# Kernel optimization log

Measured on AMD Instinct MI355X. Metric: run time of the kernel, lower is better.

## Reference

```python
import jax, jax.numpy as jnp
import numpy as np

DEPTH = 9                 # complete binary tree depth
N = 2 ** (DEPTH + 1) - 1  # 1023 nodes per tree (heap layout)
B = 32                    # batch of trees
E = 256                   # word_emb_dims
H = 512                   # treelstm in_dim (cell hidden size)
L = 512                   # decoder LSTM dims
V = 32000                 # vocab size
T = 64                    # max_sequence_length (greedy decode steps)


def setup_inputs() -> dict:
    key = jax.random.key(0)
    ks = jax.random.split(key, 12)
    g = lambda i, shape, s=0.02: jax.random.normal(ks[i], shape, jnp.float32) * s
    return {
        "node_feat": jax.random.randint(ks[0], (B, N), 0, V),
        "mask": jnp.ones((B, N), jnp.int32),
        # shared token embedding (node_emb_layer token_emb, also used by decoder input)
        "emb": g(1, (V, E)),
        # ChildSumTreeLSTMCell params (DGL convention)
        "W_iou": g(2, (E, 3 * H)),
        "U_iou": g(3, (H, 3 * H)),
        "b_iou": jnp.zeros((3 * H,), jnp.float32),
        "U_f_w": g(4, (H, H)),
        "U_f_b": jnp.zeros((H,), jnp.float32),
        # graph-readout -> decoder init state projections
        "hid_fc_w": g(5, (H, L)), "hid_fc_b": jnp.zeros((L,), jnp.float32),
        "cell_fc_w": g(6, (H, L)), "cell_fc_b": jnp.zeros((L,), jnp.float32),
        # decoder LSTMCell (PyTorch gate order i,f,g,o) + vocab projection
        "W_ih": g(7, (E, 4 * L)), "W_hh": g(8, (L, 4 * L)),
        "b_ih": jnp.zeros((4 * L,), jnp.float32), "b_hh": jnp.zeros((4 * L,), jnp.float32),
        "fc_w": g(9, (L, V)), "fc_b": jnp.zeros((V,), jnp.float32),
    }


def _forward(node_feat, mask, emb, W_iou, U_iou, b_iou, U_f_w, U_f_b,
             hid_fc_w, hid_fc_b, cell_fc_w, cell_fc_b,
             W_ih, W_hh, b_ih, b_hh, fc_w, fc_b):
    x = emb[node_feat]                                        # [B,N,E]
    iou_in = (x @ W_iou) * mask[..., None].astype(x.dtype)    # [B,N,3H]
    h = jnp.zeros((B, N, H), x.dtype)
    c = jnp.zeros((B, N, H), x.dtype)

    def apply_node(iou_node, c_agg):
        i, o, u = jnp.split(iou_node + b_iou, 3, axis=-1)
        i, o, u = jax.nn.sigmoid(i), jax.nn.sigmoid(o), jnp.tanh(u)
        c_new = i * u + c_agg
        return o * jnp.tanh(c_new), c_new

    # leaves first (no children -> zero aggregated cell)
    leaf = jnp.arange(2 ** DEPTH - 1, N)
    h_l, c_l = apply_node(iou_in[:, leaf], jnp.zeros((), x.dtype))
    h = h.at[:, leaf].set(h_l)
    c = c.at[:, leaf].set(c_l)

    # level-batched topological propagation (dgl.prop_nodes_topo)
    for d in range(DEPTH - 1, -1, -1):
        idx = jnp.arange(2 ** d - 1, 2 ** (d + 1) - 1)        # nodes at level d
        ch = jnp.stack([2 * idx + 1, 2 * idx + 2], axis=1)    # [n_d,2]
        h_ch, c_ch = h[:, ch], c[:, ch]                       # [B,n_d,2,H]
        h_tild = h_ch.sum(2)                                  # child-sum
        f = jax.nn.sigmoid(h_ch @ U_f_w + U_f_b)              # per-child forget gate
        c_agg = (f * c_ch).sum(2)
        h_n, c_n = apply_node(iou_in[:, idx] + h_tild @ U_iou, c_agg)
        h = h.at[:, idx].set(h_n)
        c = c.at[:, idx].set(c_n)

    mean_feats = h.mean(1)                                    # mean graph readout [B,H]
    hid = mean_feats @ hid_fc_w + hid_fc_b
    cel = mean_feats @ cell_fc_w + cell_fc_b

    def step(carry, _):
        inp, hs, cs = carry
        xt = emb[inp]                                         # [B,E]
        gates = xt @ W_ih + hs @ W_hh + b_ih + b_hh
        ig, fg, gg, og = jnp.split(gates, 4, axis=-1)
        cs = jax.nn.sigmoid(fg) * cs + jax.nn.sigmoid(ig) * jnp.tanh(gg)
        hs = jax.nn.sigmoid(og) * jnp.tanh(cs)
        logits = hs @ fc_w + fc_b                             # [B,V]
        top1 = jnp.argmax(logits, axis=-1)                    # greedy feedback
        return (top1, hs, cs), logits

    inp0 = jnp.zeros((B,), node_feat.dtype)
    _, logits_seq = jax.lax.scan(step, (inp0, hid, cel), None, length=T - 1)
    # t=0 row stays zeros, matching logits_output initialization
    return jnp.concatenate([jnp.zeros((1, B, V), x.dtype), logits_seq], axis=0)


def reference(node_feat, mask, emb, W_iou, U_iou, b_iou, U_f_w, U_f_b,
              hid_fc_w, hid_fc_b, cell_fc_w, cell_fc_b,
              W_ih, W_hh, b_ih, b_hh, fc_w, fc_b):
    return _forward(node_feat, mask, emb, W_iou, U_iou, b_iou, U_f_w, U_f_b,
                    hid_fc_w, hid_fc_b, cell_fc_w, cell_fc_b,
                    W_ih, W_hh, b_ih, b_hh, fc_w, fc_b)
```

## Files before the change

kernel.cpp:

```cpp
#include <hip/hip_runtime.h>
#include <math.h>

#define B_ 32
#define N_ 1023
#define E_ 256
#define H_ 512
#define V_ 32000
#define T_ 64
#define NBL 250

__device__ __forceinline__ float sigf(float x) { return 1.0f / (1.0f + expf(-x)); }

template<bool LEAF>
__global__ void __launch_bounds__(256)
iou_gemm_k(const int* __restrict__ node_feat, const int* __restrict__ mask,
           const float* __restrict__ emb, const float* __restrict__ Wiou,
           const float* __restrict__ Uiou, const float* __restrict__ hbuf,
           float* __restrict__ iou_out, int first, int n, int nshift)
{
    const int rows = B_ * n;
    const int K = LEAF ? E_ : (E_ + H_);
    const int rt = blockIdx.x, ct = blockIdx.y;
    const int tid = threadIdx.x;
    const int tr = tid >> 4, tc = tid & 15;

    __shared__ __align__(16) float As[8][136];
    __shared__ __align__(16) float Bs[8][136];

    float acc[8][8];
#pragma unroll
    for (int i = 0; i < 8; ++i)
#pragma unroll
        for (int j = 0; j < 8; ++j) acc[i][j] = 0.0f;

    const int lrow = tid >> 1;
    const int lkq  = (tid & 1) << 2;
    const int grow = rt * 128 + lrow;
    const bool rvalid = grow < rows;
    int tok = 0; float mval = 0.0f; int hoff1 = 0, hoff2 = 0;
    if (rvalid) {
        const int b = grow >> nshift, j = grow & (n - 1);
        const int node = first + j;
        tok  = node_feat[b * N_ + node];
        mval = (float)mask[b * N_ + node];
        if (!LEAF) {
            hoff1 = (b * N_ + 2 * node + 1) * H_;
            hoff2 = hoff1 + H_;
        }
    }
    const int bk   = tid >> 5;
    const int bcol = (tid & 31) << 2;
    const int gcol = ct * 128 + bcol;

    const int nkt = K >> 3;
    for (int kt = 0; kt < nkt; ++kt) {
        const int k0 = kt << 3;
        {
            const int kg = k0 + lkq;
            float4 v = make_float4(0.f, 0.f, 0.f, 0.f);
            if (rvalid) {
                if (LEAF || kg < E_) {
                    float4 e = *(const float4*)(emb + tok * E_ + kg);
                    v.x = e.x * mval; v.y = e.y * mval; v.z = e.z * mval; v.w = e.w * mval;
                } else {
                    const int kk = kg - E_;
                    float4 h1 = *(const float4*)(hbuf + hoff1 + kk);
                    float4 h2 = *(const float4*)(hbuf + hoff2 + kk);
                    v.x = h1.x + h2.x; v.y = h1.y + h2.y;
                    v.z = h1.z + h2.z; v.w = h1.w + h2.w;
                }
            }
            As[lkq + 0][lrow] = v.x;
            As[lkq + 1][lrow] = v.y;
            As[lkq + 2][lrow] = v.z;
            As[lkq + 3][lrow] = v.w;
        }
        {
            const int kg = k0 + bk;
            const float* src = (LEAF || kg < E_) ? (Wiou + kg * 1536 + gcol)
                                                 : (Uiou + (kg - E_) * 1536 + gcol);
            *(float4*)&Bs[bk][bcol] = *(const float4*)src;
        }
        __syncthreads();
#pragma unroll
        for (int kk = 0; kk < 8; ++kk) {
            float a[8], bb[8];
            *(float4*)&a[0]  = *(const float4*)&As[kk][tr << 3];
            *(float4*)&a[4]  = *(const float4*)&As[kk][(tr << 3) + 4];
            *(float4*)&bb[0] = *(const float4*)&Bs[kk][tc << 2];
            *(float4*)&bb[4] = *(const float4*)&Bs[kk][(tc << 2) + 64];
#pragma unroll
            for (int i = 0; i < 8; ++i)
#pragma unroll
                for (int j = 0; j < 8; ++j)
                    acc[i][j] = fmaf(a[i], bb[j], acc[i][j]);
        }
        __syncthreads();
    }
#pragma unroll
    for (int i = 0; i < 8; ++i) {
        const int r = rt * 128 + (tr << 3) + i;
        if (r < rows) {
            float* dst = iou_out + (size_t)r * 1536 + ct * 128;
            *(float4*)(dst + (tc << 2))      = make_float4(acc[i][0], acc[i][1], acc[i][2], acc[i][3]);
            *(float4*)(dst + 64 + (tc << 2)) = make_float4(acc[i][4], acc[i][5], acc[i][6], acc[i][7]);
        }
    }
}

__global__ void __launch_bounds__(256)
fagg_gemm_k(const float* __restrict__ hbuf, const float* __restrict__ cbuf,
            const float* __restrict__ Ufw, const float* __restrict__ Ufb,
            float* __restrict__ cagg, int first, int n, int nshift)
{
    const int rows = 64 * n;
    const int rt = blockIdx.x, ct = blockIdx.y;
    const int tid = threadIdx.x;
    const int tr = tid >> 4, tc = tid & 15;

    __shared__ __align__(16) float As[8][136];
    __shared__ __align__(16) float Bs[8][136];

    float acc[8][8];
#pragma unroll
    for (int i = 0; i < 8; ++i)
#pragma unroll
        for (int j = 0; j < 8; ++j) acc[i][j] = 0.0f;

    const int lrow = tid >> 1;
    const int lkq  = (tid & 1) << 2;
    const int grow = rt * 128 + lrow;
    const bool rvalid = grow < rows;
    int hoff = 0;
    if (rvalid) {
        const int bj = grow >> 1, s = grow & 1;
        const int b = bj >> nshift, j = bj & (n - 1);
        const int node = first + j;
        hoff = (b * N_ + 2 * node + 1 + s) * H_;
    }
    const int bk   = tid >> 5;
    const int bcol = (tid & 31) << 2;
    const int gcol = ct * 128 + bcol;

    for (int kt = 0; kt < 64; ++kt) {
        const int k0 = kt << 3;
        {
            const int kg = k0 + lkq;
            float4 v = make_float4(0.f, 0.f, 0.f, 0.f);
            if (rvalid) v = *(const float4*)(hbuf + hoff + kg);
            As[lkq + 0][lrow] = v.x;
            As[lkq + 1][lrow] = v.y;
            As[lkq + 2][lrow] = v.z;
            As[lkq + 3][lrow] = v.w;
        }
        {
            const int kg = k0 + bk;
            *(float4*)&Bs[bk][bcol] = *(const float4*)(Ufw + kg * H_ + gcol);
        }
        __syncthreads();
#pragma unroll
        for (int kk = 0; kk < 8; ++kk) {
            float a[8], bb[8];
            *(float4*)&a[0]  = *(const float4*)&As[kk][tr << 3];
            *(float4*)&a[4]  = *(const float4*)&As[kk][(tr << 3) + 4];
            *(float4*)&bb[0] = *(const float4*)&Bs[kk][tc << 2];
            *(float4*)&bb[4] = *(const float4*)&Bs[kk][(tc << 2) + 64];
#pragma unroll
            for (int i = 0; i < 8; ++i)
#pragma unroll
                for (int j = 0; j < 8; ++j)
                    acc[i][j] = fmaf(a[i], bb[j], acc[i][j]);
        }
        __syncthreads();
    }
#pragma unroll
    for (int p = 0; p < 4; ++p) {
        const int r0 = rt * 128 + (tr << 3) + 2 * p;
        if (r0 < rows) {
            const int bj = r0 >> 1;
            const int b = bj >> nshift, j = bj & (n - 1);
            const int node = first + j;
            const float* c1 = cbuf + (b * N_ + 2 * node + 1) * H_ + ct * 128;
            const float* c2 = c1 + H_;
            float* dst = cagg + bj * H_ + ct * 128;
#pragma unroll
            for (int g = 0; g < 2; ++g) {
                const int off = (g ? 64 : 0) + (tc << 2);
                const int jb = g * 4;
                float4 cc1 = *(const float4*)(c1 + off);
                float4 cc2 = *(const float4*)(c2 + off);
                float4 bbv = *(const float4*)(Ufb + ct * 128 + off);
                float4 res;
                res.x = sigf(acc[2*p][jb+0] + bbv.x) * cc1.x + sigf(acc[2*p+1][jb+0] + bbv.x) * cc2.x;
                res.y = sigf(acc[2*p][jb+1] + bbv.y) * cc1.y + sigf(acc[2*p+1][jb+1] + bbv.y) * cc2.y;
                res.z = sigf(acc[2*p][jb+2] + bbv.z) * cc1.z + sigf(acc[2*p+1][jb+2] + bbv.z) * cc2.z;
                res.w = sigf(acc[2*p][jb+3] + bbv.w) * cc1.w + sigf(acc[2*p+1][jb+3] + bbv.w) * cc2.w;
                *(float4*)(dst + off) = res;
            }
        }
    }
}

template<bool LEAF>
__global__ void apply_node_k(const float* __restrict__ iou,
                             const float* __restrict__ b_iou,
                             const float* __restrict__ cagg,
                             float* __restrict__ hbuf, float* __restrict__ cbuf,
                             int first, int n, int nshift)
{
    const int gid = blockIdx.x * 256 + threadIdx.x;
    if (gid >= B_ * n * 128) return;
    const int r = gid >> 7, col = (gid & 127) << 2;
    const float* row = iou + (size_t)r * 1536;
    float4 iv = *(const float4*)(row + col);
    float4 ov = *(const float4*)(row + 512 + col);
    float4 uv = *(const float4*)(row + 1024 + col);
    float4 bi = *(const float4*)(b_iou + col);
    float4 bo = *(const float4*)(b_iou + 512 + col);
    float4 bu = *(const float4*)(b_iou + 1024 + col);
    float4 ca = make_float4(0.f, 0.f, 0.f, 0.f);
    if (!LEAF) ca = *(const float4*)(cagg + r * H_ + col);
    float4 cn, hn;
    cn.x = sigf(iv.x + bi.x) * tanhf(uv.x + bu.x) + ca.x;
    cn.y = sigf(iv.y + bi.y) * tanhf(uv.y + bu.y) + ca.y;
    cn.z = sigf(iv.z + bi.z) * tanhf(uv.z + bu.z) + ca.z;
    cn.w = sigf(iv.w + bi.w) * tanhf(uv.w + bu.w) + ca.w;
    hn.x = sigf(ov.x + bo.x) * tanhf(cn.x);
    hn.y = sigf(ov.y + bo.y) * tanhf(cn.y);
    hn.z = sigf(ov.z + bo.z) * tanhf(cn.z);
    hn.w = sigf(ov.w + bo.w) * tanhf(cn.w);
    const int b = r >> nshift, j = r & (n - 1);
    const int node = first + j;
    const size_t o = (size_t)(b * N_ + node) * H_ + col;
    *(float4*)(cbuf + o) = cn;
    *(float4*)(hbuf + o) = hn;
}

__global__ void mean_k(const float* __restrict__ hbuf, float* __restrict__ mf)
{
    const int gid = blockIdx.x * 256 + threadIdx.x;
    const int b = gid >> 9, k = gid & 511;
    float s = 0.f;
#pragma unroll 4
    for (int nn = 0; nn < N_; ++nn) s += hbuf[(b * N_ + nn) * H_ + k];
    mf[b * H_ + k] = s * (1.0f / (float)N_);
}

__global__ void hidcel_k(const float* __restrict__ mf,
                         const float* __restrict__ hw, const float* __restrict__ hb,
                         const float* __restrict__ cw, const float* __restrict__ cb,
                         float* __restrict__ hs0, float* __restrict__ cs)
{
    const int gid = blockIdx.x * 256 + threadIdx.x;
    const int which = gid >> 14;
    const int b = (gid >> 9) & 31, l = gid & 511;
    const float* W = which ? cw : hw;
    float acc = which ? cb[l] : hb[l];
#pragma unroll 8
    for (int k = 0; k < H_; ++k) acc = fmaf(mf[b * H_ + k], W[k * H_ + l], acc);
    if (which) cs[b * H_ + l] = acc; else hs0[b * H_ + l] = acc;
}

__global__ void __launch_bounds__(256)
lstm_step_k(const float* __restrict__ emb, const float* __restrict__ W_ih,
            const float* __restrict__ W_hh, const float* __restrict__ b_ih,
            const float* __restrict__ b_hh, const float* __restrict__ pval,
            const int* __restrict__ pidx, const float* __restrict__ hs_in,
            float* __restrict__ hs_out, float* __restrict__ cs, int t)
{
    __shared__ __align__(16) float xh[768 * 32];
    __shared__ float rv[256];
    __shared__ int   ri[256];
    __shared__ int   tokS[B_];
    const int tid = threadIdx.x;

    if (t == 1) {
        if (tid < B_) tokS[tid] = 0;
    } else {
        const int b = tid & 31, ch = tid >> 5;
        float bv = -INFINITY; int bi2 = 0x7fffffff;
        for (int p = ch; p < NBL; p += 8) {
            const float v = pval[b * NBL + p];
            const int  ix = pidx[b * NBL + p];
            if (v > bv || (v == bv && ix < bi2)) { bv = v; bi2 = ix; }
        }
        rv[tid] = bv; ri[tid] = bi2;
        __syncthreads();
        if (tid < B_) {
            float Bv = -INFINITY; int Bi = 0x7fffffff;
#pragma unroll
            for (int c2 = 0; c2 < 8; ++c2) {
                const float v = rv[c2 * 32 + tid];
                const int  ix = ri[c2 * 32 + tid];
                if (v > Bv || (v == Bv && ix < Bi)) { Bv = v; Bi = ix; }
            }
            tokS[tid] = Bi;
        }
    }
    __syncthreads();

    for (int idx = tid; idx < B_ * E_; idx += 256) {
        const int b = idx >> 8, k = idx & 255;
        xh[k * 32 + b] = emb[tokS[b] * E_ + k];
    }
    for (int idx = tid; idx < B_ * H_; idx += 256) {
        const int b = idx >> 9, k = idx & 511;
        xh[(E_ + k) * 32 + b] = hs_in[b * H_ + k];
    }
    __syncthreads();

    const int b  = tid & 31;
    const int li = (tid >> 5) & 1;
    const int kq = tid >> 6;
    const int l  = blockIdx.x * 2 + li;
    float ai = 0.f, af = 0.f, ag = 0.f, ao = 0.f;
    {
        const float* w  = W_ih + (kq * 64) * 2048 + l;
        const float* xp = xh + (kq * 64) * 32 + b;
#pragma unroll 8
        for (int k = 0; k < 64; ++k) {
            const float x = xp[k * 32];
            ai = fmaf(x, w[0],    ai);
            af = fmaf(x, w[512],  af);
            ag = fmaf(x, w[1024], ag);
            ao = fmaf(x, w[1536], ao);
            w += 2048;
        }
    }
    {
        const float* w  = W_hh + (kq * 128) * 2048 + l;
        const float* xp = xh + (E_ + kq * 128) * 32 + b;
#pragma unroll 8
        for (int k = 0; k < 128; ++k) {
            const float x = xp[k * 32];
            ai = fmaf(x, w[0],    ai);
            af = fmaf(x, w[512],  af);
            ag = fmaf(x, w[1024], ag);
            ao = fmaf(x, w[1536], ao);
            w += 2048;
        }
    }
    __syncthreads();
    {
        const int slot = ((kq * 2 + li) * 32 + b) * 4;
        xh[slot + 0] = ai; xh[slot + 1] = af;
        xh[slot + 2] = ag; xh[slot + 3] = ao;
    }
    __syncthreads();
    if (tid < 64) {
        const int b2 = tid & 31, li2 = tid >> 5;
        const int l2 = blockIdx.x * 2 + li2;
        float s0 = 0.f, s1 = 0.f, s2 = 0.f, s3 = 0.f;
#pragma unroll
        for (int q = 0; q < 4; ++q) {
            const int sl = ((q * 2 + li2) * 32 + b2) * 4;
            s0 += xh[sl + 0]; s1 += xh[sl + 1];
            s2 += xh[sl + 2]; s3 += xh[sl + 3];
        }
        const float gi = s0 + b_ih[l2]        + b_hh[l2];
        const float gf = s1 + b_ih[512 + l2]  + b_hh[512 + l2];
        const float gg = s2 + b_ih[1024 + l2] + b_hh[1024 + l2];
        const float go = s3 + b_ih[1536 + l2] + b_hh[1536 + l2];
        const float co = cs[b2 * H_ + l2];
        const float cn = sigf(gf) * co + sigf(gi) * tanhf(gg);
        cs[b2 * H_ + l2] = cn;
        hs_out[b2 * H_ + l2] = sigf(go) * tanhf(cn);
    }
}

__global__ void __launch_bounds__(256)
logits_k(const float* __restrict__ fc_w, const float* __restrict__ fc_b,
         const float* __restrict__ hs, float* __restrict__ out_t,
         float* __restrict__ pval, int* __restrict__ pidx)
{
    __shared__ __align__(16) float smem[H_ * 36];
    __shared__ float rv[256];
    __shared__ int   ri[256];
    const int tid = threadIdx.x, blk = blockIdx.x;

    for (int idx = tid; idx < B_ * H_; idx += 256) {
        const int b = idx >> 9, k = idx & 511;
        smem[k * 36 + b] = hs[b * H_ + k];
    }
    __syncthreads();

    const int kq   = tid >> 6;
    const int lane = tid & 63;
    const int col  = lane << 1;
    float acc[32][2];
#pragma unroll
    for (int bb = 0; bb < 32; ++bb) { acc[bb][0] = 0.f; acc[bb][1] = 0.f; }

    const float* wp = fc_w + (size_t)(kq * 128) * V_ + blk * 128 + col;
    const float* hp = smem + (kq * 128) * 36;
#pragma unroll 4
    for (int kk = 0; kk < 128; ++kk) {
        const float2 w2 = *(const float2*)wp; wp += V_;
        float hv[16];
        *(float4*)&hv[0]  = *(const float4*)(hp + 0);
        *(float4*)&hv[4]  = *(const float4*)(hp + 4);
        *(float4*)&hv[8]  = *(const float4*)(hp + 8);
        *(float4*)&hv[12] = *(const float4*)(hp + 12);
#pragma unroll
        for (int bb = 0; bb < 16; ++bb) {
            acc[bb][0] = fmaf(hv[bb], w2.x, acc[bb][0]);
            acc[bb][1] = fmaf(hv[bb], w2.y, acc[bb][1]);
        }
        *(float4*)&hv[0]  = *(const float4*)(hp + 16);
        *(float4*)&hv[4]  = *(const float4*)(hp + 20);
        *(float4*)&hv[8]  = *(const float4*)(hp + 24);
        *(float4*)&hv[12] = *(const float4*)(hp + 28);
#pragma unroll
        for (int bb = 0; bb < 16; ++bb) {
            acc[16 + bb][0] = fmaf(hv[bb], w2.x, acc[16 + bb][0]);
            acc[16 + bb][1] = fmaf(hv[bb], w2.y, acc[16 + bb][1]);
        }
        hp += 36;
    }
    __syncthreads();

    float* redS = smem;
#pragma unroll
    for (int bb = 0; bb < 32; ++bb) {
        redS[kq * 4224 + bb * 132 + col]     = acc[bb][0];
        redS[kq * 4224 + bb * 132 + col + 1] = acc[bb][1];
    }
    __syncthreads();

    for (int idx = tid; idx < 4096; idx += 256) {
        const int c2 = idx & 127, b = idx >> 7;
        float v = redS[b * 132 + c2] + redS[4224 + b * 132 + c2]
                + redS[8448 + b * 132 + c2] + redS[12672 + b * 132 + c2]
                + fc_b[blk * 128 + c2];
        out_t[(size_t)b * V_ + blk * 128 + c2] = v;
        redS[b * 132 + c2] = v;
    }
    __syncthreads();

    {
        const int b = tid & 31, ch = tid >> 5;
        float bv = -INFINITY; int bi = 0;
#pragma unroll
        for (int j = 0; j < 16; ++j) {
            const int c2 = (ch << 4) + j;
            const float v = redS[b * 132 + c2];
            if (v > bv) { bv = v; bi = c2; }
        }
        rv[tid] = bv; ri[tid] = bi;
    }
    __syncthreads();
    if (tid < B_) {
        float bv = -INFINITY; int bi = 0;
#pragma unroll
        for (int ch = 0; ch < 8; ++ch) {
            const float v = rv[ch * 32 + tid];
            if (v > bv) { bv = v; bi = ri[ch * 32 + tid]; }
        }
        pval[tid * NBL + blk] = bv;
        pidx[tid * NBL + blk] = blk * 128 + bi;
    }
}

extern "C" void kernel_launch(void* const* d_in, const int* in_sizes, int n_in,
                              void* d_out, int out_size, void* d_ws, size_t ws_size,
                              hipStream_t stream)
{
    (void)in_sizes; (void)n_in; (void)out_size; (void)ws_size;
    const int*   node_feat = (const int*)  d_in[0];
    const int*   mask      = (const int*)  d_in[1];
    const float* emb       = (const float*)d_in[2];
    const float* W_iou     = (const float*)d_in[3];
    const float* U_iou     = (const float*)d_in[4];
    const float* b_iou     = (const float*)d_in[5];
    const float* U_f_w     = (const float*)d_in[6];
    const float* U_f_b     = (const float*)d_in[7];
    const float* hid_fc_w  = (const float*)d_in[8];
    const float* hid_fc_b  = (const float*)d_in[9];
    const float* cell_fc_w = (const float*)d_in[10];
    const float* cell_fc_b = (const float*)d_in[11];
    const float* W_ih      = (const float*)d_in[12];
    const float* W_hh      = (const float*)d_in[13];
    const float* b_ih      = (const float*)d_in[14];
    const float* b_hh      = (const float*)d_in[15];
    const float* fc_w      = (const float*)d_in[16];
    const float* fc_b      = (const float*)d_in[17];
    float* out = (float*)d_out;

    float* ws      = (float*)d_ws;
    float* iou_buf = ws;
    float* cagg    = ws + 12582912;
    float* hbuf    = ws + 16777216;
    float* cbuf    = ws + 33538048;
    float* mf      = ws + 50298880;
    float* hsb     = ws + 50315264;
    float* csb     = ws + 50348032;
    float* pval    = ws + 50364416;
    int*   pidx    = (int*)(ws + 50372416);

    for (int chunk = 0; chunk < 2; ++chunk) {
        const int first = 511 + 256 * chunk;
        dim3 g(64, 12);
        iou_gemm_k<true><<<g, 256, 0, stream>>>(node_feat, mask, emb, W_iou, U_iou,
                                                hbuf, iou_buf, first, 256, 8);
        apply_node_k<true><<<4096, 256, 0, stream>>>(iou_buf, b_iou, cagg,
                                                     hbuf, cbuf, first, 256, 8);
    }
    for (int d = 8; d >= 0; --d) {
        const int n = 1 << d, first = n - 1;
        dim3 gf((64 * n + 127) / 128, 4);
        fagg_gemm_k<<<gf, 256, 0, stream>>>(hbuf, cbuf, U_f_w, U_f_b, cagg, first, n, d);
        dim3 gi((32 * n + 127) / 128, 12);
        iou_gemm_k<false><<<gi, 256, 0, stream>>>(node_feat, mask, emb, W_iou, U_iou,
                                                  hbuf, iou_buf, first, n, d);
        apply_node_k<false><<<16 * n, 256, 0, stream>>>(iou_buf, b_iou, cagg,
                                                        hbuf, cbuf, first, n, d);
    }
    mean_k<<<64, 256, 0, stream>>>(hbuf, mf);
    hidcel_k<<<128, 256, 0, stream>>>(mf, hid_fc_w, hid_fc_b, cell_fc_w, cell_fc_b, hsb, csb);
    hipMemsetAsync(d_out, 0, (size_t)B_ * V_ * sizeof(float), stream);
    for (int t = 1; t < T_; ++t) {
        const float* hs_in  = hsb + ((t - 1) & 1) * (B_ * H_);
        float*       hs_out = hsb + (t & 1) * (B_ * H_);
        lstm_step_k<<<256, 256, 0, stream>>>(emb, W_ih, W_hh, b_ih, b_hh,
                                             pval, pidx, hs_in, hs_out, csb, t);
        logits_k<<<NBL, 256, 0, stream>>>(fc_w, fc_b, hs_out,
                                          out + (size_t)t * B_ * V_, pval, pidx);
    }
}
```

Baseline: 6.560 ms.

## Fuse decoder loop into persistent kernel with grid barriers; add small-tile tree GEMMs

```diff
diff --git a/kernel.cpp b/kernel.cpp
--- a/kernel.cpp
+++ b/kernel.cpp
@@ -8,8 +8,23 @@
 #define V_ 32000
 #define T_ 64
 #define NBL 250
+#define DECB 256
 
 __device__ __forceinline__ float sigf(float x) { return 1.0f / (1.0f + expf(-x)); }
+
+__device__ __forceinline__ void gridbar(unsigned* c)
+{
+    __syncthreads();
+    if (threadIdx.x == 0) {
+        __threadfence();
+        __hip_atomic_fetch_add(c, 1u, __ATOMIC_ACQ_REL, __HIP_MEMORY_SCOPE_AGENT);
+        while (__hip_atomic_load(c, __ATOMIC_ACQUIRE, __HIP_MEMORY_SCOPE_AGENT) < (unsigned)DECB) {
+            __builtin_amdgcn_s_sleep(2);
+        }
+        __threadfence();
+    }
+    __syncthreads();
+}
 
 template<bool LEAF>
 __global__ void __launch_bounds__(256)
@@ -109,6 +124,91 @@
 }
 
 __global__ void __launch_bounds__(256)
+iou_small_k(const int* __restrict__ node_feat, const int* __restrict__ mask,
+            const float* __restrict__ emb, const float* __restrict__ Wiou,
+            const float* __restrict__ Uiou, const float* __restrict__ hbuf,
+            float* __restrict__ iou_out, int first, int n, int nshift)
+{
+    const int rows = B_ * n;
+    const int rt = blockIdx.x, ct = blockIdx.y;
+    const int tid = threadIdx.x;
+    const int tr = tid >> 4, tc = tid & 15;
+
+    __shared__ __align__(16) float As[8][72];
+    __shared__ __align__(16) float Bs[8][72];
+
+    float acc[4][4];
+#pragma unroll
+    for (int i = 0; i < 4; ++i)
+#pragma unroll
+        for (int j = 0; j < 4; ++j) acc[i][j] = 0.0f;
+
+    const int srow = tid & 63, skq = tid >> 6;
+    const int grow = rt * 64 + srow;
+    const bool rvalid = grow < rows;
+    int tok = 0; float mval = 0.f; int hoff1 = 0, hoff2 = 0;
+    if (rvalid) {
+        const int b = grow >> nshift, j = grow & (n - 1);
+        const int node = first + j;
+        tok  = node_feat[b * N_ + node];
+        mval = (float)mask[b * N_ + node];
+        hoff1 = (b * N_ + 2 * node + 1) * H_;
+        hoff2 = hoff1 + H_;
+    }
+    const int gcol = ct * 64 + srow;
+
+    for (int kt = 0; kt < 96; ++kt) {
+        const int k0 = kt << 3;
+        {
+            const int kg = k0 + (skq << 1);
+            float2 v = make_float2(0.f, 0.f);
+            if (rvalid) {
+                if (kg < E_) {
+                    float2 e = *(const float2*)(emb + tok * E_ + kg);
+                    v.x = e.x * mval; v.y = e.y * mval;
+                } else {
+                    const int kk = kg - E_;
+                    float2 h1 = *(const float2*)(hbuf + hoff1 + kk);
+                    float2 h2 = *(const float2*)(hbuf + hoff2 + kk);
+                    v.x = h1.x + h2.x; v.y = h1.y + h2.y;
+                }
+            }
+            As[(skq << 1) + 0][srow] = v.x;
+            As[(skq << 1) + 1][srow] = v.y;
+        }
+        {
+            const int kg = k0 + (skq << 1);
+            const float* s0 = (kg < E_) ? (Wiou + (size_t)kg * 1536 + gcol)
+                                        : (Uiou + (size_t)(kg - E_) * 1536 + gcol);
+            const float* s1 = ((kg + 1) < E_) ? (Wiou + (size_t)(kg + 1) * 1536 + gcol)
+                                              : (Uiou + (size_t)(kg + 1 - E_) * 1536 + gcol);
+            Bs[(skq << 1) + 0][srow] = *s0;
+            Bs[(skq << 1) + 1][srow] = *s1;
+        }
+        __syncthreads();
+#pragma unroll
+        for (int kk = 0; kk < 8; ++kk) {
+            float a[4], bb[4];
+            *(float4*)&a[0]  = *(const float4*)&As[kk][tr << 2];
+            *(float4*)&bb[0] = *(const float4*)&Bs[kk][tc << 2];
+#pragma unroll
+            for (int i = 0; i < 4; ++i)
+#pragma unroll
+                for (int j = 0; j < 4; ++j)
+                    acc[i][j] = fmaf(a[i], bb[j], acc[i][j]);
+        }
+        __syncthreads();
+    }
+#pragma unroll
+    for (int i = 0; i < 4; ++i) {
+        const int r = rt * 64 + (tr << 2) + i;
+        if (r < rows)
+            *(float4*)(iou_out + (size_t)r * 1536 + ct * 64 + (tc << 2)) =
+                make_float4(acc[i][0], acc[i][1], acc[i][2], acc[i][3]);
+    }
+}
+
+__global__ void __launch_bounds__(256)
 fagg_gemm_k(const float* __restrict__ hbuf, const float* __restrict__ cbuf,
             const float* __restrict__ Ufw, const float* __restrict__ Ufb,
             float* __restrict__ cagg, int first, int n, int nshift)
@@ -197,6 +297,89 @@
                 res.w = sigf(acc[2*p][jb+3] + bbv.w) * cc1.w + sigf(acc[2*p+1][jb+3] + bbv.w) * cc2.w;
                 *(float4*)(dst + off) = res;
             }
+        }
+    }
+}
+
+__global__ void __launch_bounds__(256)
+fagg_small_k(const float* __restrict__ hbuf, const float* __restrict__ cbuf,
+             const float* __restrict__ Ufw, const float* __restrict__ Ufb,
+             float* __restrict__ cagg, int first, int n, int nshift)
+{
+    const int rows = 64 * n;
+    const int rt = blockIdx.x, ct = blockIdx.y;
+    const int tid = threadIdx.x;
+    const int tr = tid >> 4, tc = tid & 15;
+
+    __shared__ __align__(16) float As[8][72];
+    __shared__ __align__(16) float Bs[8][72];
+
+    float acc[4][4];
+#pragma unroll
+    for (int i = 0; i < 4; ++i)
+#pragma unroll
+        for (int j = 0; j < 4; ++j) acc[i][j] = 0.0f;
+
+    const int srow = tid & 63, skq = tid >> 6;
+    const int grow = rt * 64 + srow;
+    const bool rvalid = grow < rows;
+    int hoff = 0;
+    if (rvalid) {
+        const int bj = grow >> 1, s = grow & 1;
+        const int b = bj >> nshift, j = bj & (n - 1);
+        const int node = first + j;
+        hoff = (b * N_ + 2 * node + 1 + s) * H_;
+    }
+    const int gcol = ct * 64 + srow;
+
+    for (int kt = 0; kt < 64; ++kt) {
+        const int k0 = kt << 3;
+        {
+            const int kg = k0 + (skq << 1);
+            float2 v = make_float2(0.f, 0.f);
+            if (rvalid) v = *(const float2*)(hbuf + hoff + kg);
+            As[(skq << 1) + 0][srow] = v.x;
+            As[(skq << 1) + 1][srow] = v.y;
+        }
+        {
+            const int kg = k0 + (skq << 1);
+            Bs[(skq << 1) + 0][srow] = Ufw[(size_t)kg * H_ + gcol];
+            Bs[(skq << 1) + 1][srow] = Ufw[(size_t)(kg + 1) * H_ + gcol];
+        }
+        __syncthreads();
+#pragma unroll
+        for (int kk = 0; kk < 8; ++kk) {
+            float a[4], bb[4];
+            *(float4*)&a[0]  = *(const float4*)&As[kk][tr << 2];
+            *(float4*)&bb[0] = *(const float4*)&Bs[kk][tc << 2];
+#pragma unroll
+            for (int i = 0; i < 4; ++i)
+#pragma unroll
+                for (int j = 0; j < 4; ++j)
+                    acc[i][j] = fmaf(a[i], bb[j], acc[i][j]);
+        }
+        __syncthreads();
+    }
+#pragma unroll
+    for (int p = 0; p < 2; ++p) {
+        const int r0 = rt * 64 + (tr << 2) + 2 * p;
+        if (r0 < rows) {
+            const int bj = r0 >> 1;
+            const int b = bj >> nshift, j = bj & (n - 1);
+            const int node = first + j;
+            const float* c1 = cbuf + (b * N_ + 2 * node + 1) * H_ + ct * 64;
+            const float* c2 = c1 + H_;
+            float* dst = cagg + bj * H_ + ct * 64;
+            const int off = tc << 2;
+            float4 cc1 = *(const float4*)(c1 + off);
+            float4 cc2 = *(const float4*)(c2 + off);
+            float4 bbv = *(const float4*)(Ufb + ct * 64 + off);
+            float4 res;
+            res.x = sigf(acc[2*p][0] + bbv.x) * cc1.x + sigf(acc[2*p+1][0] + bbv.x) * cc2.x;
+            res.y = sigf(acc[2*p][1] + bbv.y) * cc1.y + sigf(acc[2*p+1][1] + bbv.y) * cc2.y;
+            res.z = sigf(acc[2*p][2] + bbv.z) * cc1.z + sigf(acc[2*p+1][2] + bbv.z) * cc2.z;
+            res.w = sigf(acc[2*p][3] + bbv.w) * cc1.w + sigf(acc[2*p+1][3] + bbv.w) * cc2.w;
+            *(float4*)(dst + off) = res;
         }
     }
 }
@@ -236,14 +419,31 @@
     *(float4*)(hbuf + o) = hn;
 }
 
-__global__ void mean_k(const float* __restrict__ hbuf, float* __restrict__ mf)
+__global__ void mean_part_k(const float* __restrict__ hbuf, float* __restrict__ mpart)
+{
+    const int bid = blockIdx.x;
+    const int b = bid >> 3, chunk = bid & 7;
+    const int tid = threadIdx.x;
+    const int n0 = chunk * 128;
+    const int n1 = (n0 + 128 < N_) ? (n0 + 128) : N_;
+    float s0 = 0.f, s1 = 0.f;
+    for (int nn = n0; nn < n1; ++nn) {
+        const float* p = hbuf + (size_t)(b * N_ + nn) * H_;
+        s0 += p[tid];
+        s1 += p[tid + 256];
+    }
+    mpart[(bid << 9) + tid]       = s0;
+    mpart[(bid << 9) + tid + 256] = s1;
+}
+
+__global__ void mean_fin_k(const float* __restrict__ mpart, float* __restrict__ mf)
 {
     const int gid = blockIdx.x * 256 + threadIdx.x;
     const int b = gid >> 9, k = gid & 511;
     float s = 0.f;
-#pragma unroll 4
-    for (int nn = 0; nn < N_; ++nn) s += hbuf[(b * N_ + nn) * H_ + k];
-    mf[b * H_ + k] = s * (1.0f / (float)N_);
+#pragma unroll
+    for (int c = 0; c < 8; ++c) s += mpart[(((b << 3) + c) << 9) + k];
+    mf[gid] = s * (1.0f / 1023.0f);
 }
 
 __global__ void hidcel_k(const float* __restrict__ mf,
@@ -262,202 +462,206 @@
 }
 
 __global__ void __launch_bounds__(256)
-lstm_step_k(const float* __restrict__ emb, const float* __restrict__ W_ih,
-            const float* __restrict__ W_hh, const float* __restrict__ b_ih,
-            const float* __restrict__ b_hh, const float* __restrict__ pval,
-            const int* __restrict__ pidx, const float* __restrict__ hs_in,
-            float* __restrict__ hs_out, float* __restrict__ cs, int t)
-{
-    __shared__ __align__(16) float xh[768 * 32];
+decoder_k(const float* __restrict__ emb, const float* __restrict__ W_ih,
+          const float* __restrict__ W_hh, const float* __restrict__ b_ih,
+          const float* __restrict__ b_hh, const float* __restrict__ fc_w,
+          const float* __restrict__ fc_b, float* __restrict__ hsb,
+          float* __restrict__ csb, float* __restrict__ out,
+          float* __restrict__ pval, int* __restrict__ pidx, unsigned* bar)
+{
+    __shared__ __align__(16) float sh[24576];
     __shared__ float rv[256];
     __shared__ int   ri[256];
     __shared__ int   tokS[B_];
-    const int tid = threadIdx.x;
-
-    if (t == 1) {
-        if (tid < B_) tokS[tid] = 0;
-    } else {
-        const int b = tid & 31, ch = tid >> 5;
-        float bv = -INFINITY; int bi2 = 0x7fffffff;
-        for (int p = ch; p < NBL; p += 8) {
-            const float v = pval[b * NBL + p];
-            const int  ix = pidx[b * NBL + p];
-            if (v > bv || (v == bv && ix < bi2)) { bv = v; bi2 = ix; }
-        }
-        rv[tid] = bv; ri[tid] = bi2;
-        __syncthreads();
-        if (tid < B_) {
-            float Bv = -INFINITY; int Bi = 0x7fffffff;
-#pragma unroll
-            for (int c2 = 0; c2 < 8; ++c2) {
-                const float v = rv[c2 * 32 + tid];
-                const int  ix = ri[c2 * 32 + tid];
-                if (v > Bv || (v == Bv && ix < Bi)) { Bv = v; Bi = ix; }
-            }
-            tokS[tid] = Bi;
-        }
-    }
-    __syncthreads();
-
-    for (int idx = tid; idx < B_ * E_; idx += 256) {
-        const int b = idx >> 8, k = idx & 255;
-        xh[k * 32 + b] = emb[tokS[b] * E_ + k];
-    }
-    for (int idx = tid; idx < B_ * H_; idx += 256) {
-        const int b = idx >> 9, k = idx & 511;
-        xh[(E_ + k) * 32 + b] = hs_in[b * H_ + k];
-    }
-    __syncthreads();
-
-    const int b  = tid & 31;
-    const int li = (tid >> 5) & 1;
-    const int kq = tid >> 6;
-    const int l  = blockIdx.x * 2 + li;
-    float ai = 0.f, af = 0.f, ag = 0.f, ao = 0.f;
-    {
-        const float* w  = W_ih + (kq * 64) * 2048 + l;
-        const float* xp = xh + (kq * 64) * 32 + b;
+    const int bid = blockIdx.x, tid = threadIdx.x;
+
+    for (int t = 1; t < T_; ++t) {
+        const float* hs_in  = hsb + ((t - 1) & 1) * (B_ * H_);
+        float*       hs_out = hsb + (t & 1) * (B_ * H_);
+
+        if (t == 1) {
+            if (tid < B_) tokS[tid] = 0;
+        } else {
+            const int b = tid & 31, ch = tid >> 5;
+            float bv = -INFINITY; int bi2 = 0x7fffffff;
+            for (int p = ch; p < NBL; p += 8) {
+                const float v = pval[b * NBL + p];
+                const int  ix = pidx[b * NBL + p];
+                if (v > bv || (v == bv && ix < bi2)) { bv = v; bi2 = ix; }
+            }
+            rv[tid] = bv; ri[tid] = bi2;
+            __syncthreads();
+            if (tid < B_) {
+                float Bv = -INFINITY; int Bi = 0x7fffffff;
+#pragma unroll
+                for (int c2 = 0; c2 < 8; ++c2) {
+                    const float v = rv[c2 * 32 + tid];
+                    const int  ix = ri[c2 * 32 + tid];
+                    if (v > Bv || (v == Bv && ix < Bi)) { Bv = v; Bi = ix; }
+                }
+                tokS[tid] = Bi;
+            }
+        }
+        __syncthreads();
+
+        for (int idx = tid; idx < B_ * E_; idx += 256) {
+            const int b = idx >> 8, k = idx & 255;
+            sh[k * 32 + b] = emb[tokS[b] * E_ + k];
+        }
+        for (int idx = tid; idx < B_ * H_; idx += 256) {
+            const int b = idx >> 9, k = idx & 511;
+            sh[(E_ + k) * 32 + b] = hs_in[b * H_ + k];
+        }
+        __syncthreads();
+
+        {
+            const int b  = tid & 31;
+            const int li = (tid >> 5) & 1;
+            const int kq = tid >> 6;
+            const int l  = bid * 2 + li;
+            float ai = 0.f, af = 0.f, ag = 0.f, ao = 0.f;
+            {
+                const float* w  = W_ih + (kq * 64) * 2048 + l;
+                const float* xp = sh + (kq * 64) * 32 + b;
 #pragma unroll 8
-        for (int k = 0; k < 64; ++k) {
-            const float x = xp[k * 32];
-            ai = fmaf(x, w[0],    ai);
-            af = fmaf(x, w[512],  af);
-            ag = fmaf(x, w[1024], ag);
-            ao = fmaf(x, w[1536], ao);
-            w += 2048;
-        }
-    }
-    {
-        const float* w  = W_hh + (kq * 128) * 2048 + l;
-        const float* xp = xh + (E_ + kq * 128) * 32 + b;
+                for (int k = 0; k < 64; ++k) {
+                    const float x = xp[k * 32];
+                    ai = fmaf(x, w[0],    ai);
+                    af = fmaf(x, w[512],  af);
+                    ag = fmaf(x, w[1024], ag);
+                    ao = fmaf(x, w[1536], ao);
+                    w += 2048;
+                }
+            }
+            {
+                const float* w  = W_hh + (kq * 128) * 2048 + l;
+                const float* xp = sh + (E_ + kq * 128) * 32 + b;
 #pragma unroll 8
-        for (int k = 0; k < 128; ++k) {
-            const float x = xp[k * 32];
-            ai = fmaf(x, w[0],    ai);
-            af = fmaf(x, w[512],  af);
-            ag = fmaf(x, w[1024], ag);
-            ao = fmaf(x, w[1536], ao);
-            w += 2048;
-        }
-    }
-    __syncthreads();
-    {
-        const int slot = ((kq * 2 + li) * 32 + b) * 4;
-        xh[slot + 0] = ai; xh[slot + 1] = af;
-        xh[slot + 2] = ag; xh[slot + 3] = ao;
-    }
-    __syncthreads();
-    if (tid < 64) {
-        const int b2 = tid & 31, li2 = tid >> 5;
-        const int l2 = blockIdx.x * 2 + li2;
-        float s0 = 0.f, s1 = 0.f, s2 = 0.f, s3 = 0.f;
-#pragma unroll
-        for (int q = 0; q < 4; ++q) {
-            const int sl = ((q * 2 + li2) * 32 + b2) * 4;
-            s0 += xh[sl + 0]; s1 += xh[sl + 1];
-            s2 += xh[sl + 2]; s3 += xh[sl + 3];
-        }
-        const float gi = s0 + b_ih[l2]        + b_hh[l2];
-        const float gf = s1 + b_ih[512 + l2]  + b_hh[512 + l2];
-        const float gg = s2 + b_ih[1024 + l2] + b_hh[1024 + l2];
-        const float go = s3 + b_ih[1536 + l2] + b_hh[1536 + l2];
-        const float co = cs[b2 * H_ + l2];
-        const float cn = sigf(gf) * co + sigf(gi) * tanhf(gg);
-        cs[b2 * H_ + l2] = cn;
-        hs_out[b2 * H_ + l2] = sigf(go) * tanhf(cn);
-    }
-}
-
-__global__ void __launch_bounds__(256)
-logits_k(const float* __restrict__ fc_w, const float* __restrict__ fc_b,
-         const float* __restrict__ hs, float* __restrict__ out_t,
-         float* __restrict__ pval, int* __restrict__ pidx)
-{
-    __shared__ __align__(16) float smem[H_ * 36];
-    __shared__ float rv[256];
-    __shared__ int   ri[256];
-    const int tid = threadIdx.x, blk = blockIdx.x;
-
-    for (int idx = tid; idx < B_ * H_; idx += 256) {
-        const int b = idx >> 9, k = idx & 511;
-        smem[k * 36 + b] = hs[b * H_ + k];
-    }
-    __syncthreads();
-
-    const int kq   = tid >> 6;
-    const int lane = tid & 63;
-    const int col  = lane << 1;
-    float acc[32][2];
-#pragma unroll
-    for (int bb = 0; bb < 32; ++bb) { acc[bb][0] = 0.f; acc[bb][1] = 0.f; }
-
-    const float* wp = fc_w + (size_t)(kq * 128) * V_ + blk * 128 + col;
-    const float* hp = smem + (kq * 128) * 36;
-#pragma unroll 4
-    for (int kk = 0; kk < 128; ++kk) {
-        const float2 w2 = *(const float2*)wp; wp += V_;
-        float hv[16];
-        *(float4*)&hv[0]  = *(const float4*)(hp + 0);
-        *(float4*)&hv[4]  = *(const float4*)(hp + 4);
-        *(float4*)&hv[8]  = *(const float4*)(hp + 8);
-        *(float4*)&hv[12] = *(const float4*)(hp + 12);
-#pragma unroll
-        for (int bb = 0; bb < 16; ++bb) {
-            acc[bb][0] = fmaf(hv[bb], w2.x, acc[bb][0]);
-            acc[bb][1] = fmaf(hv[bb], w2.y, acc[bb][1]);
-        }
-        *(float4*)&hv[0]  = *(const float4*)(hp + 16);
-        *(float4*)&hv[4]  = *(const float4*)(hp + 20);
-        *(float4*)&hv[8]  = *(const float4*)(hp + 24);
-        *(float4*)&hv[12] = *(const float4*)(hp + 28);
-#pragma unroll
-        for (int bb = 0; bb < 16; ++bb) {
-            acc[16 + bb][0] = fmaf(hv[bb], w2.x, acc[16 + bb][0]);
-            acc[16 + bb][1] = fmaf(hv[bb], w2.y, acc[16 + bb][1]);
-        }
-        hp += 36;
-    }
-    __syncthreads();
-
-    float* redS = smem;
-#pragma unroll
-    for (int bb = 0; bb < 32; ++bb) {
-        redS[kq * 4224 + bb * 132 + col]     = acc[bb][0];
-        redS[kq * 4224 + bb * 132 + col + 1] = acc[bb][1];
-    }
-    __syncthreads();
-
-    for (int idx = tid; idx < 4096; idx += 256) {
-        const int c2 = idx & 127, b = idx >> 7;
-        float v = redS[b * 132 + c2] + redS[4224 + b * 132 + c2]
-                + redS[8448 + b * 132 + c2] + redS[12672 + b * 132 + c2]
-                + fc_b[blk * 128 + c2];
-        out_t[(size_t)b * V_ + blk * 128 + c2] = v;
-        redS[b * 132 + c2] = v;
-    }
-    __syncthreads();
-
-    {
-        const int b = tid & 31, ch = tid >> 5;
-        float bv = -INFINITY; int bi = 0;
-#pragma unroll
-        for (int j = 0; j < 16; ++j) {
-            const int c2 = (ch << 4) + j;
-            const float v = redS[b * 132 + c2];
-            if (v > bv) { bv = v; bi = c2; }
-        }
-        rv[tid] = bv; ri[tid] = bi;
-    }
-    __syncthreads();
-    if (tid < B_) {
-        float bv = -INFINITY; int bi = 0;
-#pragma unroll
-        for (int ch = 0; ch < 8; ++ch) {
-            const float v = rv[ch * 32 + tid];
-            if (v > bv) { bv = v; bi = ri[ch * 32 + tid]; }
-        }
-        pval[tid * NBL + blk] = bv;
-        pidx[tid * NBL + blk] = blk * 128 + bi;
+                for (int k = 0; k < 128; ++k) {
+                    const float x = xp[k * 32];
+                    ai = fmaf(x, w[0],    ai);
+                    af = fmaf(x, w[512],  af);
+                    ag = fmaf(x, w[1024], ag);
+                    ao = fmaf(x, w[1536], ao);
+                    w += 2048;
+                }
+            }
+            __syncthreads();
+            {
+                const int slot = ((kq * 2 + li) * 32 + b) * 4;
+                sh[slot + 0] = ai; sh[slot + 1] = af;
+                sh[slot + 2] = ag; sh[slot + 3] = ao;
+            }
+            __syncthreads();
+            if (tid < 64) {
+                const int b2 = tid & 31, li2 = tid >> 5;
+                const int l2 = bid * 2 + li2;
+                float s0 = 0.f, s1 = 0.f, s2 = 0.f, s3 = 0.f;
+#pragma unroll
+                for (int q = 0; q < 4; ++q) {
+                    const int sl = ((q * 2 + li2) * 32 + b2) * 4;
+                    s0 += sh[sl + 0]; s1 += sh[sl + 1];
+                    s2 += sh[sl + 2]; s3 += sh[sl + 3];
+                }
+                const float gi = s0 + b_ih[l2]        + b_hh[l2];
+                const float gf = s1 + b_ih[512 + l2]  + b_hh[512 + l2];
+                const float gg = s2 + b_ih[1024 + l2] + b_hh[1024 + l2];
+                const float go = s3 + b_ih[1536 + l2] + b_hh[1536 + l2];
+                const float co = csb[b2 * H_ + l2];
+                const float cn = sigf(gf) * co + sigf(gi) * tanhf(gg);
+                csb[b2 * H_ + l2] = cn;
+                hs_out[b2 * H_ + l2] = sigf(go) * tanhf(cn);
+            }
+        }
+        gridbar(bar + 2 * t - 2);
+
+        if (bid < NBL) {
+            for (int idx = tid; idx < B_ * H_; idx += 256) {
+                const int b = idx >> 9, k = idx & 511;
+                sh[k * 36 + b] = hs_out[b * H_ + k];
+            }
+            __syncthreads();
+
+            const int kq = tid >> 6, lane = tid & 63;
+            const int col = lane << 1;
+            float acc[32][2];
+#pragma unroll
+            for (int bb = 0; bb < 32; ++bb) { acc[bb][0] = 0.f; acc[bb][1] = 0.f; }
+
+            const float* wp = fc_w + (size_t)(kq * 128) * V_ + bid * 128 + col;
+            const float* hp = sh + (kq * 128) * 36;
+            float2 wreg[8];
+#pragma unroll
+            for (int j = 0; j < 8; ++j) wreg[j] = *(const float2*)(wp + (size_t)j * V_);
+            for (int kb = 0; kb < 16; ++kb) {
+                float2 wnxt[8];
+                if (kb < 15) {
+                    const float* wq = wp + (size_t)((kb + 1) << 3) * V_;
+#pragma unroll
+                    for (int j = 0; j < 8; ++j) wnxt[j] = *(const float2*)(wq + (size_t)j * V_);
+                }
+#pragma unroll
+                for (int j = 0; j < 8; ++j) {
+                    const float* hq = hp + ((kb << 3) + j) * 36;
+                    float hv[32];
+#pragma unroll
+                    for (int q = 0; q < 8; ++q)
+                        *(float4*)&hv[q << 2] = *(const float4*)(hq + (q << 2));
+#pragma unroll
+                    for (int bb = 0; bb < 32; ++bb) {
+                        acc[bb][0] = fmaf(hv[bb], wreg[j].x, acc[bb][0]);
+                        acc[bb][1] = fmaf(hv[bb], wreg[j].y, acc[bb][1]);
+                    }
+                }
+                if (kb < 15) {
+#pragma unroll
+                    for (int j = 0; j < 8; ++j) wreg[j] = wnxt[j];
+                }
+            }
+            __syncthreads();
+
+            float* redS = sh;
+#pragma unroll
+            for (int bb = 0; bb < 32; ++bb) {
+                redS[kq * 4224 + bb * 132 + col]     = acc[bb][0];
+                redS[kq * 4224 + bb * 132 + col + 1] = acc[bb][1];
+            }
+            __syncthreads();
+
+            float* out_t = out + (size_t)t * (B_ * V_);
+            for (int idx = tid; idx < 4096; idx += 256) {
+                const int c2 = idx & 127, b = idx >> 7;
+                float v = redS[b * 132 + c2] + redS[4224 + b * 132 + c2]
+                        + redS[8448 + b * 132 + c2] + redS[12672 + b * 132 + c2]
+                        + fc_b[bid * 128 + c2];
+                out_t[(size_t)b * V_ + bid * 128 + c2] = v;
+                redS[b * 132 + c2] = v;
+            }
+            __syncthreads();
+            {
+                const int b = tid & 31, ch = tid >> 5;
+                float bv = -INFINITY; int bi = 0;
+#pragma unroll
+                for (int j = 0; j < 16; ++j) {
+                    const int c2 = (ch << 4) + j;
+                    const float v = redS[b * 132 + c2];
+                    if (v > bv) { bv = v; bi = c2; }
+                }
+                rv[tid] = bv; ri[tid] = bi;
+            }
+            __syncthreads();
+            if (tid < B_) {
+                float bv = -INFINITY; int bi = 0;
+#pragma unroll
+                for (int ch = 0; ch < 8; ++ch) {
+                    const float v = rv[ch * 32 + tid];
+                    if (v > bv) { bv = v; bi = ri[ch * 32 + tid]; }
+                }
+                pval[tid * NBL + bid] = bv;
+                pidx[tid * NBL + bid] = bid * 128 + bi;
+            }
+        }
+        gridbar(bar + 2 * t - 1);
     }
 }
 
@@ -496,6 +700,8 @@
     float* csb     = ws + 50348032;
     float* pval    = ws + 50364416;
     int*   pidx    = (int*)(ws + 50372416);
+    float*    mpart = iou_buf;
+    unsigned* bar   = (unsigned*)(iou_buf + 131072);
 
     for (int chunk = 0; chunk < 2; ++chunk) {
         const int first = 511 + 256 * chunk;
@@ -507,23 +713,27 @@
     }
     for (int d = 8; d >= 0; --d) {
         const int n = 1 << d, first = n - 1;
-        dim3 gf((64 * n + 127) / 128, 4);
-        fagg_gemm_k<<<gf, 256, 0, stream>>>(hbuf, cbuf, U_f_w, U_f_b, cagg, first, n, d);
-        dim3 gi((32 * n + 127) / 128, 12);
-        iou_gemm_k<false><<<gi, 256, 0, stream>>>(node_feat, mask, emb, W_iou, U_iou,
-                                                  hbuf, iou_buf, first, n, d);
+        if (n <= 64) {
+            dim3 gf((64 * n + 63) / 64, 8);
+            fagg_small_k<<<gf, 256, 0, stream>>>(hbuf, cbuf, U_f_w, U_f_b, cagg, first, n, d);
+            dim3 gi((32 * n + 63) / 64, 24);
+            iou_small_k<<<gi, 256, 0, stream>>>(node_feat, mask, emb, W_iou, U_iou,
+                                                hbuf, iou_buf, first, n, d);
+        } else {
+            dim3 gf((64 * n + 127) / 128, 4);
+            fagg_gemm_k<<<gf, 256, 0, stream>>>(hbuf, cbuf, U_f_w, U_f_b, cagg, first, n, d);
+            dim3 gi((32 * n + 127) / 128, 12);
+            iou_gemm_k<false><<<gi, 256, 0, stream>>>(node_feat, mask, emb, W_iou, U_iou,
+                                                      hbuf, iou_buf, first, n, d);
+        }
         apply_node_k<false><<<16 * n, 256, 0, stream>>>(iou_buf, b_iou, cagg,
                                                         hbuf, cbuf, first, n, d);
     }
-    mean_k<<<64, 256, 0, stream>>>(hbuf, mf);
+    hipMemsetAsync(bar, 0, 128 * sizeof(unsigned), stream);
+    mean_part_k<<<256, 256, 0, stream>>>(hbuf, mpart);
+    mean_fin_k<<<64, 256, 0, stream>>>(mpart, mf);
     hidcel_k<<<128, 256, 0, stream>>>(mf, hid_fc_w, hid_fc_b, cell_fc_w, cell_fc_b, hsb, csb);
     hipMemsetAsync(d_out, 0, (size_t)B_ * V_ * sizeof(float), stream);
-    for (int t = 1; t < T_; ++t) {
-        const float* hs_in  = hsb + ((t - 1) & 1) * (B_ * H_);
-        float*       hs_out = hsb + (t & 1) * (B_ * H_);
-        lstm_step_k<<<256, 256, 0, stream>>>(emb, W_ih, W_hh, b_ih, b_hh,
-                                             pval, pidx, hs_in, hs_out, csb, t);
-        logits_k<<<NBL, 256, 0, stream>>>(fc_w, fc_b, hs_out,
-                                          out + (size_t)t * B_ * V_, pval, pidx);
-    }
-}
+    decoder_k<<<DECB, 256, 0, stream>>>(emb, W_ih, W_hh, b_ih, b_hh, fc_w, fc_b,
+                                        hsb, csb, out, pval, pidx, bar);
+}
```

After: 8.795 ms. +34.1%, slower.
